# Kernel optimization log

Hardware: AMD Instinct MI355X
Metric: run time of the kernel (lower is better)

## Reference

```python
import jax, jax.numpy as jnp
import numpy as np

B, NZ, NX, NT, NR = 4, 256, 256, 256, 128
DT, DH, OMEGA = 1e-3, 10.0, 10.0  # time step [s], grid spacing [m], SLS reference angular freq


def setup_inputs() -> dict:
    key = jax.random.key(0)
    ks = jax.random.split(key, 6)
    x = jax.random.normal(ks[0], (B, NT, 1), jnp.float32)          # source wavelet per shot
    vp = 1500.0 + 2000.0 * jax.random.uniform(ks[1], (NZ, NX), jnp.float32)   # m/s
    rho = 1000.0 + 1000.0 * jax.random.uniform(ks[2], (NZ, NX), jnp.float32)  # kg/m^3
    Q = 20.0 + 80.0 * jax.random.uniform(ks[3], (NZ, NX), jnp.float32)        # quality factor
    src_z = jnp.full((B,), 2, jnp.int32)
    src_x = jax.random.randint(ks[4], (B,), 0, NX).astype(jnp.int32)
    rec_x = jnp.sort(jax.random.randint(ks[5], (NR,), 0, NX)).astype(jnp.int32)
    rec_z = 2
    return {"x": x, "vp": vp, "rho": rho, "Q": Q,
            "src_z": src_z, "src_x": src_x, "rec_x": rec_x, "rec_z": rec_z}


def _dxb(p):  # backward difference along x
    return (p - jnp.pad(p, ((0, 0), (0, 0), (1, 0)))[:, :, :-1]) / DH

def _dzb(p):
    return (p - jnp.pad(p, ((0, 0), (1, 0), (0, 0)))[:, :-1, :]) / DH

def _dxf(v):  # forward difference along x
    return (jnp.pad(v, ((0, 0), (0, 0), (0, 1)))[:, :, 1:] - v) / DH

def _dzf(v):
    return (jnp.pad(v, ((0, 0), (0, 1), (0, 0)))[:, 1:, :] - v) / DH


def reference(x, vp, rho, Q, src_z, src_x, rec_x, rec_z):
    kappa = rho * vp * vp                  # bulk modulus [NZ, NX]
    tau = 1.0 / Q                          # SLS attenuation level
    tau_sigma = 1.0 / OMEGA                # stress relaxation time
    ca = 1.0 - DT / (2.0 * tau_sigma)
    cb = 1.0 + DT / (2.0 * tau_sigma)
    bidx = jnp.arange(B)

    def step(carry, xi):                   # xi: [B] wavelet amplitude at this step
        vx, vz, p, r = carry
        vx = vx - (DT / rho) * _dxb(p)
        vz = vz - (DT / rho) * _dzb(p)
        div = _dxf(vx) + _dzf(vz)
        r = (ca * r - (DT / tau_sigma) * kappa * tau * div) / cb   # memory variable
        p = p - DT * kappa * (1.0 + tau) * div + DT * r
        p = p.at[bidx, src_z, src_x].add(xi)                       # source injection
        rec = p[:, rec_z, :][:, rec_x]                             # probe readout [B, NR]
        return (vx, vz, p, r), rec

    z = jnp.zeros((B, NZ, NX), x.dtype)
    wav = jnp.transpose(x[:, :, 0])        # [NT, B]
    _, recs = jax.lax.scan(step, (z, z, z, z), wav)  # recs: [NT, B, NR]
    return jnp.transpose(recs, (0, 2, 1))  # [NT, NR, B], matching stack(dim=1).permute(1,2,0)
```

## Files before the change

### kernel.cpp

```cpp
#include <hip/hip_runtime.h>

namespace {
constexpr int NZ = 256, NX = 256, NT = 256, NR = 128, B = 4;
constexpr int K = 8;
constexpr int OROWS = 4;
constexpr int IROWS = OROWS + 2 * K;
constexpr int NSTRIP = 4;
constexpr int RPT = IROWS / NSTRIP;
constexpr int ZB = NZ / OROWS;
constexpr int NBLK = B * ZB;
constexpr int NL = NT / K;
constexpr int NXCD = 8;
constexpr int CHUNK = NBLK / NXCD;
constexpr float DT = 1e-3f, DH = 10.0f, OMEGA = 10.0f;
constexpr float TS  = 1.0f / OMEGA;
constexpr float CBv = 1.0f + DT / (2.0f * TS);
constexpr float CA  = (1.0f - DT / (2.0f * TS)) / CBv;

__device__ inline float dpp_shr1(float v) {
  int r = __builtin_amdgcn_update_dpp(0, __builtin_bit_cast(int, v),
                                      0x138, 0xF, 0xF, false);
  return __builtin_bit_cast(float, r);
}
__device__ inline float dpp_shl1(float v) {
  int r = __builtin_amdgcn_update_dpp(0, __builtin_bit_cast(int, v),
                                      0x130, 0xF, 0xF, false);
  return __builtin_bit_cast(float, r);
}
}

__global__ void coef_kernel(const float* __restrict__ vp, const float* __restrict__ rho,
                            const float* __restrict__ Q, float4* __restrict__ cf) {
  int i = blockIdx.x * blockDim.x + threadIdx.x;
  if (i >= NZ * NX) return;
  float v = vp[i], rh = rho[i], q = Q[i];
  float kappa = rh * v * v, tau = 1.0f / q;
  cf[i] = make_float4(DT / (rh * DH), DT * kappa * tau / (TS * CBv * DH),
                      DT * kappa * (1.0f + tau) / DH, 0.0f);
}

__global__ __launch_bounds__(1024, 4) void step_fused(
    const float4* __restrict__ Sin, float4* __restrict__ Sout,
    const float4* __restrict__ Cf, const float* __restrict__ wav,
    const int* __restrict__ src_z, const int* __restrict__ src_x,
    const int* __restrict__ rec_x, const int* __restrict__ rec_z,
    float* __restrict__ out, int t0)
{
  const int tid  = threadIdx.x;
  const int x    = tid & (NX - 1);
  const int g    = tid >> 8;
  const int lane = x & 63;
  const int wx   = x >> 6;
  const int j0   = g * RPT;
  const int lbid = (blockIdx.x & (NXCD - 1)) * CHUNK + (blockIdx.x >> 3);
  const int b    = lbid / ZB, zb = lbid % ZB;
  const int z0   = zb * OROWS;
  const int zi0  = z0 - K;
  const size_t base = (size_t)b * NZ * NX;

  __shared__ float pse[NSTRIP][NX];
  __shared__ float vze[NSTRIP][NX];
  __shared__ float pxe[NSTRIP][4][RPT];
  __shared__ float vxe_s[NSTRIP][4][RPT];
  __shared__ float prow[NX];
  __shared__ float wav_s[K];
  __shared__ int   rx_s[NR];

  float pr[RPT], vxr[RPT], vz[RPT], rr[RPT], a1[RPT], b2[RPT], b3[RPT];

  #pragma unroll
  for (int jj = 0; jj < RPT; ++jj) {
    int gz = zi0 + j0 + jj;
    bool in = (unsigned)gz < (unsigned)NZ;
    float4 st = in ? Sin[base + (size_t)gz * NX + x] : make_float4(0, 0, 0, 0);
    float4 cf = in ? Cf[(size_t)gz * NX + x]        : make_float4(0, 0, 0, 0);
    pr[jj] = st.x; vxr[jj] = st.y; vz[jj] = st.z; rr[jj] = st.w;
    a1[jj] = cf.x; b2[jj] = cf.y; b3[jj] = cf.z;
  }
  pse[g][x] = pr[RPT - 1];
  if (wx < 3 && lane == 63) {
    #pragma unroll
    for (int jj = 0; jj < RPT; ++jj) pxe[g][wx][jj] = pr[jj];
  }
  if (tid < NR) rx_s[tid] = rec_x[tid];
  if (tid < K)  wav_s[tid] = wav[b * NT + t0 + tid];
  const int sz = src_z[b], sx = src_x[b];
  const int rz = rec_z[0];
  const bool owner = (rz >= z0 && rz < z0 + OROWS);
  const int jrow = rz - zi0;
  __syncthreads();

  for (int s = 0; s < K; ++s) {
    float pu0 = (g > 0) ? pse[g - 1][x] : 0.0f;
    float ple[RPT] = {0, 0, 0, 0, 0};
    if (wx > 0 && lane == 0) {
      #pragma unroll
      for (int jj = 0; jj < RPT; ++jj) ple[jj] = pxe[g][wx - 1][jj];
    }
    #pragma unroll
    for (int jj = 0; jj < RPT; ++jj) {
      float pc = pr[jj];
      float pl = dpp_shr1(pc);
      if (lane == 0) pl = ple[jj];
      float pu = jj ? pr[jj - 1] : pu0;
      vxr[jj] -= a1[jj] * (pc - pl);
      vz[jj]  -= a1[jj] * (pc - pu);
    }
    vze[g][x] = vz[0];
    if (wx > 0 && lane == 0) {
      #pragma unroll
      for (int jj = 0; jj < RPT; ++jj) vxe_s[g][wx][jj] = vxr[jj];
    }
    __syncthreads();

    float vzb_ = (g < NSTRIP - 1) ? vze[g + 1][x] : 0.0f;
    float vxe[RPT] = {0, 0, 0, 0, 0};
    if (wx < 3 && lane == 63) {
      #pragma unroll
      for (int jj = 0; jj < RPT; ++jj) vxe[jj] = vxe_s[g][wx + 1][jj];
    }
    const float xi = wav_s[s];
    #pragma unroll
    for (int jj = 0; jj < RPT; ++jj) {
      float vxR = dpp_shl1(vxr[jj]);
      if (lane == 63) vxR = vxe[jj];
      float vzn = (jj < RPT - 1) ? vz[jj + 1] : vzb_;
      float div = (vxR - vxr[jj]) + (vzn - vz[jj]);
      float rn = CA * rr[jj] - b2[jj] * div;
      rr[jj] = rn;
      float pn = pr[jj] - b3[jj] * div + DT * rn;
      if (zi0 + j0 + jj == sz && x == sx) pn += xi;
      pr[jj] = pn;
    }
    pse[g][x] = pr[RPT - 1];
    if (wx < 3 && lane == 63) {
      #pragma unroll
      for (int jj = 0; jj < RPT; ++jj) pxe[g][wx][jj] = pr[jj];
    }
    if (owner) {
      #pragma unroll
      for (int jj = 0; jj < RPT; ++jj)
        if (j0 + jj == jrow) prow[x] = pr[jj];
    }
    __syncthreads();
    if (owner && tid < NR)
      out[(size_t)(t0 + s) * NR * B + (size_t)tid * B + b] = prow[rx_s[tid]];
  }

  #pragma unroll
  for (int jj = 0; jj < RPT; ++jj) {
    int j = j0 + jj;
    if (j >= K && j < K + OROWS)
      Sout[base + (size_t)(zi0 + j) * NX + x] =
          make_float4(pr[jj], vxr[jj], vz[jj], rr[jj]);
  }
}

extern "C" void kernel_launch(void* const* d_in, const int* in_sizes, int n_in,
                              void* d_out, int out_size, void* d_ws, size_t ws_size,
                              hipStream_t stream) {
  const float* xw  = (const float*)d_in[0];
  const float* vp  = (const float*)d_in[1];
  const float* rho = (const float*)d_in[2];
  const float* Q   = (const float*)d_in[3];
  const int* src_z = (const int*)d_in[4];
  const int* src_x = (const int*)d_in[5];
  const int* rec_x = (const int*)d_in[6];
  const int* rec_z = (const int*)d_in[7];
  float* out = (float*)d_out;

  const size_t S = (size_t)B * NZ * NX;
  float4* s0 = (float4*)d_ws;
  float4* s1 = s0 + S;
  float4* cf = s1 + S;

  hipMemsetAsync(s0, 0, S * sizeof(float4), stream);
  coef_kernel<<<(NZ * NX + 255) / 256, 256, 0, stream>>>(vp, rho, Q, cf);

  for (int l = 0; l < NL; ++l) {
    float4* in   = (l & 1) ? s1 : s0;
    float4* out4 = (l & 1) ? s0 : s1;
    step_fused<<<NBLK, 1024, 0, stream>>>(in, out4, cf, xw, src_z, src_x,
                                          rec_x, rec_z, out, l * K);
  }
}
```

Measured before the change: 371.6 us.

## Replicate neighbor velocity updates to drop mid-step barrier, double-buffer halos

Each strip and wavefront-edge lane now keeps a shadow copy of the neighbouring vz/vx values and their coefficients, and recomputes the neighbour's velocity update from exchanged pressure halos (top and bottom rows, left and right columns). This removes the second __syncthreads per time step and the velocity halo exchange. Pressure halo buffers are double-buffered by step parity so one barrier per step is enough. The cost is redundant arithmetic, extra initial global loads, and more registers and shared memory.

```diff
diff --git a/kernel.cpp b/kernel.cpp
--- a/kernel.cpp
+++ b/kernel.cpp
@@ -58,15 +58,17 @@
   const int zi0  = z0 - K;
   const size_t base = (size_t)b * NZ * NX;
 
-  __shared__ float pse[NSTRIP][NX];
-  __shared__ float vze[NSTRIP][NX];
-  __shared__ float pxe[NSTRIP][4][RPT];
-  __shared__ float vxe_s[NSTRIP][4][RPT];
-  __shared__ float prow[NX];
+  __shared__ float pse[2][NSTRIP][NX];
+  __shared__ float pte[2][NSTRIP][NX];
+  __shared__ float pxe [2][NSTRIP][3][RPT];
+  __shared__ float pxe0[2][NSTRIP][3][RPT];
+  __shared__ float prow[2][NX];
   __shared__ float wav_s[K];
   __shared__ int   rx_s[NR];
 
   float pr[RPT], vxr[RPT], vz[RPT], rr[RPT], a1[RPT], b2[RPT], b3[RPT];
+  float vx_sh[RPT], a1_r[RPT];
+  float vz_sh, a1_sh;
 
   #pragma unroll
   for (int jj = 0; jj < RPT; ++jj) {
@@ -76,11 +78,35 @@
     float4 cf = in ? Cf[(size_t)gz * NX + x]        : make_float4(0, 0, 0, 0);
     pr[jj] = st.x; vxr[jj] = st.y; vz[jj] = st.z; rr[jj] = st.w;
     a1[jj] = cf.x; b2[jj] = cf.y; b3[jj] = cf.z;
-  }
-  pse[g][x] = pr[RPT - 1];
-  if (wx < 3 && lane == 63) {
-    #pragma unroll
-    for (int jj = 0; jj < RPT; ++jj) pxe[g][wx][jj] = pr[jj];
+    vx_sh[jj] = 0.0f; a1_r[jj] = 0.0f;
+  }
+  vz_sh = 0.0f; a1_sh = 0.0f;
+  if (g < NSTRIP - 1) {
+    int gz = zi0 + j0 + RPT;
+    if ((unsigned)gz < (unsigned)NZ) {
+      vz_sh = Sin[base + (size_t)gz * NX + x].z;
+      a1_sh = Cf[(size_t)gz * NX + x].x;
+    }
+  }
+  if (lane == 63 && wx < 3) {
+    #pragma unroll
+    for (int jj = 0; jj < RPT; ++jj) {
+      int gz = zi0 + j0 + jj;
+      if ((unsigned)gz < (unsigned)NZ) {
+        vx_sh[jj] = Sin[base + (size_t)gz * NX + x + 1].y;
+        a1_r[jj]  = Cf[(size_t)gz * NX + x + 1].x;
+      }
+    }
+  }
+  pse[0][g][x] = pr[RPT - 1];
+  pte[0][g][x] = pr[0];
+  if (lane == 63 && wx < 3) {
+    #pragma unroll
+    for (int jj = 0; jj < RPT; ++jj) pxe[0][g][wx][jj] = pr[jj];
+  }
+  if (lane == 0 && wx > 0) {
+    #pragma unroll
+    for (int jj = 0; jj < RPT; ++jj) pxe0[0][g][wx - 1][jj] = pr[jj];
   }
   if (tid < NR) rx_s[tid] = rec_x[tid];
   if (tid < K)  wav_s[tid] = wav[b * NT + t0 + tid];
@@ -91,11 +117,18 @@
   __syncthreads();
 
   for (int s = 0; s < K; ++s) {
-    float pu0 = (g > 0) ? pse[g - 1][x] : 0.0f;
+    const int par = s & 1, nxt = par ^ 1;
+    float pu0 = (g > 0) ? pse[par][g - 1][x] : 0.0f;
+    float pbt = (g < NSTRIP - 1) ? pte[par][g + 1][x] : 0.0f;
     float ple[RPT] = {0, 0, 0, 0, 0};
-    if (wx > 0 && lane == 0) {
-      #pragma unroll
-      for (int jj = 0; jj < RPT; ++jj) ple[jj] = pxe[g][wx - 1][jj];
+    float prt[RPT] = {0, 0, 0, 0, 0};
+    if (lane == 0 && wx > 0) {
+      #pragma unroll
+      for (int jj = 0; jj < RPT; ++jj) ple[jj] = pxe[par][g][wx - 1][jj];
+    }
+    if (lane == 63 && wx < 3) {
+      #pragma unroll
+      for (int jj = 0; jj < RPT; ++jj) prt[jj] = pxe0[par][g][wx][jj];
     }
     #pragma unroll
     for (int jj = 0; jj < RPT; ++jj) {
@@ -106,25 +139,19 @@
       vxr[jj] -= a1[jj] * (pc - pl);
       vz[jj]  -= a1[jj] * (pc - pu);
     }
-    vze[g][x] = vz[0];
-    if (wx > 0 && lane == 0) {
-      #pragma unroll
-      for (int jj = 0; jj < RPT; ++jj) vxe_s[g][wx][jj] = vxr[jj];
-    }
-    __syncthreads();
-
-    float vzb_ = (g < NSTRIP - 1) ? vze[g + 1][x] : 0.0f;
-    float vxe[RPT] = {0, 0, 0, 0, 0};
-    if (wx < 3 && lane == 63) {
-      #pragma unroll
-      for (int jj = 0; jj < RPT; ++jj) vxe[jj] = vxe_s[g][wx + 1][jj];
-    }
+    vz_sh -= a1_sh * (pbt - pr[RPT - 1]);
+    if (lane == 63 && wx < 3) {
+      #pragma unroll
+      for (int jj = 0; jj < RPT; ++jj)
+        vx_sh[jj] -= a1_r[jj] * (prt[jj] - pr[jj]);
+    }
+
     const float xi = wav_s[s];
     #pragma unroll
     for (int jj = 0; jj < RPT; ++jj) {
       float vxR = dpp_shl1(vxr[jj]);
-      if (lane == 63) vxR = vxe[jj];
-      float vzn = (jj < RPT - 1) ? vz[jj + 1] : vzb_;
+      if (lane == 63) vxR = vx_sh[jj];
+      float vzn = (jj < RPT - 1) ? vz[jj + 1] : vz_sh;
       float div = (vxR - vxr[jj]) + (vzn - vz[jj]);
       float rn = CA * rr[jj] - b2[jj] * div;
       rr[jj] = rn;
@@ -132,19 +159,26 @@
       if (zi0 + j0 + jj == sz && x == sx) pn += xi;
       pr[jj] = pn;
     }
-    pse[g][x] = pr[RPT - 1];
-    if (wx < 3 && lane == 63) {
-      #pragma unroll
-      for (int jj = 0; jj < RPT; ++jj) pxe[g][wx][jj] = pr[jj];
+
+    pse[nxt][g][x] = pr[RPT - 1];
+    pte[nxt][g][x] = pr[0];
+    if (lane == 63 && wx < 3) {
+      #pragma unroll
+      for (int jj = 0; jj < RPT; ++jj) pxe[nxt][g][wx][jj] = pr[jj];
+    }
+    if (lane == 0 && wx > 0) {
+      #pragma unroll
+      for (int jj = 0; jj < RPT; ++jj) pxe0[nxt][g][wx - 1][jj] = pr[jj];
     }
     if (owner) {
       #pragma unroll
       for (int jj = 0; jj < RPT; ++jj)
-        if (j0 + jj == jrow) prow[x] = pr[jj];
+        if (j0 + jj == jrow) prow[par][x] = pr[jj];
     }
     __syncthreads();
     if (owner && tid < NR)
-      out[(size_t)(t0 + s) * NR * B + (size_t)tid * B + b] = prow[rx_s[tid]];
+      out[(size_t)(t0 + s) * NR * B + (size_t)tid * B + b] =
+          prow[par][rx_s[tid]];
   }
 
   #pragma unroll
```

Result: slower. 405.0 us (+9.0%).
